# Kernel optimization log

Hardware: AMD Instinct MI355X
Metric: run time of the kernel (lower is better)

Reference implementation:

```python
import jax, jax.numpy as jnp
import numpy as np

N_GRIDS = 16
N_FEATS = 2
GRID_SHAPE = (64, 64, 64)  # D, H, W
NODES = 64
N_OUT = 1
DATA_MIN = 0.0
DATA_MAX = 1.0
N_POINTS = 524288


def setup_inputs() -> dict:
    key = jax.random.key(0)
    ks = jax.random.split(key, 12)
    x = jax.random.uniform(ks[0], (N_POINTS, 3), jnp.float32, -1.0, 1.0)
    # matches randomize_grids(): scales ~ log(1 - U*0.05), rotations ~ identity quat + noise,
    # translations ~ U(-0.05, 0.05)
    scales = jnp.log(1.0 - jax.random.uniform(ks[1], (N_GRIDS, 3), jnp.float32) * 0.05)
    rotations = jnp.zeros((N_GRIDS, 4), jnp.float32).at[:, 3].set(1.0) \
        + jax.random.normal(ks[2], (N_GRIDS, 4), jnp.float32) * 0.05
    translations = jax.random.uniform(ks[3], (N_GRIDS, 3), jnp.float32) * 0.1 - 0.05
    # original uses U(-1e-4, 1e-4); use a larger scale for numerically meaningful outputs
    feature_grids = jax.random.uniform(ks[4], (N_GRIDS, N_FEATS) + GRID_SHAPE,
                                       jnp.float32, -0.1, 0.1)
    d_in = N_GRIDS * N_FEATS
    def xavier(k, fi, fo):
        std = np.sqrt(2.0 / (fi + fo)).astype(np.float32)
        return jax.random.normal(k, (fi, fo), jnp.float32) * std
    W0 = xavier(ks[5], d_in, NODES)
    b0 = jax.random.normal(ks[6], (NODES,), jnp.float32) * 0.001
    W1 = xavier(ks[7], NODES, NODES)
    b1 = jax.random.normal(ks[8], (NODES,), jnp.float32) * 0.001
    W2 = xavier(ks[9], NODES, N_OUT)
    b2 = jax.random.normal(ks[10], (N_OUT,), jnp.float32) * 0.001
    return {"x": x, "rotations": rotations, "scales": scales,
            "translations": translations, "feature_grids": feature_grids,
            "W0": W0, "b0": b0, "W1": W1, "b1": b1, "W2": W2, "b2": b2}


def quat_to_rot(q):
    # q: [G,4] in (x, y, z, w) order; normalized (rotation_activation)
    q = q / jnp.linalg.norm(q, axis=-1, keepdims=True)
    x, y, z, w = q[:, 0], q[:, 1], q[:, 2], q[:, 3]
    r0 = jnp.stack([1 - 2 * (y * y + z * z), 2 * (x * y - z * w), 2 * (x * z + y * w)], -1)
    r1 = jnp.stack([2 * (x * y + z * w), 1 - 2 * (x * x + z * z), 2 * (y * z - x * w)], -1)
    r2 = jnp.stack([2 * (x * z - y * w), 2 * (y * z + x * w), 1 - 2 * (x * x + y * y)], -1)
    return jnp.stack([r0, r1, r2], axis=-2)  # [G,3,3]


def transform_points(x, rotations, scales, translations):
    # S*R*T order: local = diag(exp(scales)) @ R @ x + t, per grid -> [G,N,3]
    R = quat_to_rot(rotations)
    s = jnp.exp(scales)
    M = s[:, :, None] * R  # [G,3,3]
    return jnp.einsum('gij,nj->gni', M, x) + translations[:, None, :]


def trilinear_sample(grid, pts):
    # grid: [C,D,H,W]; pts: [N,3] (x,y,z) in [-1,1]; grid_sample semantics:
    # mode='bilinear', align_corners=True, padding_mode='zeros'
    C, D, H, W = grid.shape
    fx = (pts[:, 0] + 1.0) * 0.5 * (W - 1)
    fy = (pts[:, 1] + 1.0) * 0.5 * (H - 1)
    fz = (pts[:, 2] + 1.0) * 0.5 * (D - 1)
    x0 = jnp.floor(fx); y0 = jnp.floor(fy); z0 = jnp.floor(fz)
    wx = fx - x0; wy = fy - y0; wz = fz - z0
    x0i = x0.astype(jnp.int32); y0i = y0.astype(jnp.int32); z0i = z0.astype(jnp.int32)

    def corner(dx, dy, dz):
        xi = x0i + dx; yi = y0i + dy; zi = z0i + dz
        valid = (xi >= 0) & (xi < W) & (yi >= 0) & (yi < H) & (zi >= 0) & (zi < D)
        v = grid[:, jnp.clip(zi, 0, D - 1), jnp.clip(yi, 0, H - 1), jnp.clip(xi, 0, W - 1)]
        w = ((wx if dx else 1 - wx) * (wy if dy else 1 - wy) * (wz if dz else 1 - wz))
        return v * jnp.where(valid, w, 0.0)[None, :]

    out = corner(0, 0, 0)
    for dz in (0, 1):
        for dy in (0, 1):
            for dx in (0, 1):
                if (dx, dy, dz) != (0, 0, 0):
                    out = out + corner(dx, dy, dz)
    return out  # [C,N]


def reference(x, rotations, scales, translations, feature_grids, W0, b0, W1, b1, W2, b2):
    pts = transform_points(x, rotations, scales, translations)      # [G,N,3]
    feats = jax.vmap(trilinear_sample)(feature_grids, pts)          # [G,C,N]
    feats = feats.transpose(2, 0, 1).reshape(x.shape[0], -1)        # [N, G*C]
    h = jax.nn.relu(feats @ W0 + b0)
    h = jax.nn.relu(h @ W1 + b1)
    y = h @ W2 + b2
    return y * (DATA_MAX - DATA_MIN) + DATA_MIN
```

## Files before the change

### kernel.cpp

```cpp
#include <hip/hip_runtime.h>
#include <cstddef>
#include <cstdint>

constexpr int NPTS   = 524288;
constexpr int NG     = 16;
constexpr int GR     = 64;
constexpr int GR3    = GR * GR * GR;
constexpr int NNODES = 64;
constexpr int NBINS  = 32768;

constexpr size_t GRIDS_BYTES = (size_t)NG * GR3 * 8;
constexpr size_t WS_SORT     = GRIDS_BYTES;
constexpr size_t SORT_BYTES  = (size_t)NPTS * 16;
constexpr size_t WS_KEYR     = WS_SORT + SORT_BYTES;
constexpr size_t KEYR_BYTES  = (size_t)NPTS * 4;
constexpr size_t WS_BINS     = WS_KEYR + KEYR_BYTES;
constexpr size_t BINS_BYTES  = (size_t)NBINS * 4;
constexpr size_t WS_MATS     = WS_BINS + BINS_BYTES;
constexpr size_t MATS_BYTES  = 1024;
constexpr size_t WS_WPACK    = WS_MATS + MATS_BYTES;
constexpr size_t WPACK_BYTES = (size_t)(256 + 512) * 16;
constexpr size_t WS_PART     = WS_WPACK + WPACK_BYTES;
constexpr size_t PART_BYTES  = 128 * 4;
constexpr size_t WS_TOTAL    = WS_PART + PART_BYTES;

constexpr int PREP_REPACK = 4096;
constexpr int PREP_HIST   = 2048;

typedef _Float16 half8 __attribute__((ext_vector_type(8)));
typedef float    floatx4 __attribute__((ext_vector_type(4)));

__device__ __forceinline__ unsigned part1by2(unsigned x) {
    x &= 0x3ff;
    x = (x | (x << 16)) & 0x030000FF;
    x = (x | (x <<  8)) & 0x0300F00F;
    x = (x | (x <<  4)) & 0x030C30C3;
    x = (x | (x <<  2)) & 0x09249249;
    return x;
}

__device__ __forceinline__ unsigned cell_of(float px, float py, float pz) {
    int cx = (int)((px + 1.0f) * 16.0f); cx = min(max(cx, 0), 31);
    int cy = (int)((py + 1.0f) * 16.0f); cy = min(max(cy, 0), 31);
    int cz = (int)((pz + 1.0f) * 16.0f); cz = min(max(cz, 0), 31);
    return part1by2((unsigned)cx) | (part1by2((unsigned)cy) << 1) | (part1by2((unsigned)cz) << 2);
}

__device__ __forceinline__ unsigned f32_to_bf16_rne(float f) {
    unsigned u = __float_as_uint(f);
    return (u + 0x7fffu + ((u >> 16) & 1u)) >> 16;
}

__device__ __forceinline__ unsigned pack_h2(float a, float b) {
    unsigned short ua = __builtin_bit_cast(unsigned short, (_Float16)a);
    unsigned short ub = __builtin_bit_cast(unsigned short, (_Float16)b);
    return (unsigned)ua | ((unsigned)ub << 16);
}

__device__ __forceinline__ unsigned short f32_to_h16(float a) {
    return __builtin_bit_cast(unsigned short, (_Float16)a);
}

__global__ __launch_bounds__(256) void prep_kernel(
    const float* __restrict__ grids, uint2* __restrict__ gout,
    const float* __restrict__ xs, unsigned* __restrict__ bins,
    unsigned* __restrict__ keyrank,
    const float* __restrict__ rot, const float* __restrict__ scl,
    const float* __restrict__ trn, float* __restrict__ mats,
    const float* __restrict__ W0, const float* __restrict__ W1,
    uint4* __restrict__ wpack)
{
    const int bid = blockIdx.x;
    const int tid = threadIdx.x;

    if (bid < PREP_REPACK) {
        const int base = (bid * 256 + tid) * 4;
        const int g    = base >> 18;
        const int node = base & (GR3 - 1);
        const int x    = node & 63;
        const float* p0 = grids + (size_t)g * 2 * GR3 + node;
        const float* p1 = p0 + GR3;
        const float4 c0 = *(const float4*)p0;
        const float4 c1 = *(const float4*)p1;
        float d0n, d1n;
        if (x == 60) { d0n = c0.w; d1n = c1.w; }
        else         { d0n = p0[4]; d1n = p1[4]; }
        const float e0[5] = {c0.x, c0.y, c0.z, c0.w, d0n};
        const float e1[5] = {c1.x, c1.y, c1.z, c1.w, d1n};
        unsigned pk[5];
        #pragma unroll
        for (int i = 0; i < 5; ++i)
            pk[i] = f32_to_bf16_rne(e0[i]) | (f32_to_bf16_rne(e1[i]) << 16);
        uint4* dst = (uint4*)(gout + (size_t)g * GR3 + node);
        dst[0] = make_uint4(pk[0], pk[1], pk[1], pk[2]);
        dst[1] = make_uint4(pk[2], pk[3], pk[3], pk[4]);
    } else if (bid < PREP_REPACK + PREP_HIST) {
        const int n = (bid - PREP_REPACK) * 256 + tid;
        const unsigned key = cell_of(xs[n*3+0], xs[n*3+1], xs[n*3+2]);
        const unsigned rank = atomicAdd(&bins[key], 1u);
        keyrank[n] = key | (rank << 15);
    } else if (bid == PREP_REPACK + PREP_HIST) {
        const int g = tid;
        if (g < NG) {
            float qx = rot[g*4+0], qy = rot[g*4+1], qz = rot[g*4+2], qw = rot[g*4+3];
            const float inv = 1.0f / sqrtf(qx*qx + qy*qy + qz*qz + qw*qw);
            qx *= inv; qy *= inv; qz *= inv; qw *= inv;
            const float sx = expf(scl[g*3+0]);
            const float sy = expf(scl[g*3+1]);
            const float sz = expf(scl[g*3+2]);
            float* m = mats + g * 12;
            m[0] = sx * (1.0f - 2.0f*(qy*qy + qz*qz));
            m[1] = sx * (2.0f*(qx*qy - qz*qw));
            m[2] = sx * (2.0f*(qx*qz + qy*qw));
            m[3] = sy * (2.0f*(qx*qy + qz*qw));
            m[4] = sy * (1.0f - 2.0f*(qx*qx + qz*qz));
            m[5] = sy * (2.0f*(qy*qz - qx*qw));
            m[6] = sz * (2.0f*(qx*qz - qy*qw));
            m[7] = sz * (2.0f*(qy*qz + qx*qw));
            m[8] = sz * (1.0f - 2.0f*(qx*qx + qy*qy));
            m[9]  = trn[g*3+0];
            m[10] = trn[g*3+1];
            m[11] = trn[g*3+2];
        }
    } else {
        const int t = tid >> 6;
        const int lane = tid & 63;
        const int q = lane >> 4, c = lane & 15;
        const int n = t * 16 + c;
        {
            unsigned u[4];
            #pragma unroll
            for (int jj = 0; jj < 4; ++jj) {
                const int k0 = q * 8 + 2 * jj;
                u[jj] = pack_h2(W0[k0 * NNODES + n], W0[(k0 + 1) * NNODES + n]);
            }
            wpack[t * 64 + lane] = make_uint4(u[0], u[1], u[2], u[3]);
        }
        #pragma unroll
        for (int ks = 0; ks < 2; ++ks) {
            unsigned u[4];
            #pragma unroll
            for (int jj = 0; jj < 4; ++jj) {
                const int k0 = ks * 32 + q * 8 + 2 * jj;
                u[jj] = pack_h2(W1[k0 * NNODES + n], W1[(k0 + 1) * NNODES + n]);
            }
            wpack[256 + (ks * 4 + t) * 64 + lane] = make_uint4(u[0], u[1], u[2], u[3]);
        }
    }
}

__global__ __launch_bounds__(256) void scanA_kernel(unsigned* __restrict__ bins,
                                                    unsigned* __restrict__ part) {
    __shared__ unsigned s[256];
    const int t = threadIdx.x;
    const int base = blockIdx.x * 256;
    const unsigned v = bins[base + t];
    s[t] = v;
    __syncthreads();
    for (int off = 1; off < 256; off <<= 1) {
        unsigned u = (t >= off) ? s[t - off] : 0u;
        __syncthreads();
        s[t] += u;
        __syncthreads();
    }
    bins[base + t] = s[t] - v;
    if (t == 255) part[blockIdx.x] = s[255];
}

__global__ __launch_bounds__(128) void scanB_kernel(unsigned* __restrict__ part) {
    __shared__ unsigned s[128];
    const int t = threadIdx.x;
    const unsigned v = part[t];
    s[t] = v;
    __syncthreads();
    for (int off = 1; off < 128; off <<= 1) {
        unsigned u = (t >= off) ? s[t - off] : 0u;
        __syncthreads();
        s[t] += u;
        __syncthreads();
    }
    part[t] = s[t] - v;
}

__global__ __launch_bounds__(256) void scatter_kernel(const float* __restrict__ xs,
                                                      const unsigned* __restrict__ bins,
                                                      const unsigned* __restrict__ part,
                                                      const unsigned* __restrict__ keyrank,
                                                      float4* __restrict__ sorted) {
    const int n = blockIdx.x * 256 + threadIdx.x;
    if (n >= NPTS) return;
    const unsigned kr = keyrank[n];
    const unsigned key = kr & 0x7fffu;
    const unsigned rank = kr >> 15;
    const unsigned pos = part[key >> 8] + bins[key] + rank;
    sorted[pos] = make_float4(xs[n*3+0], xs[n*3+1], xs[n*3+2], __int_as_float(n));
}

struct Geom {
    unsigned i00, i01, i10, i11;
    float ax0, ax1, ay0, ay1, az0, az1;
};

__device__ __forceinline__ Geom make_geom(const float* __restrict__ m,
                                          float px, float py, float pz, int g) {
    Geom G;
    const float tx = fmaf(m[0], px, fmaf(m[1], py, fmaf(m[2], pz, m[9])));
    const float ty = fmaf(m[3], px, fmaf(m[4], py, fmaf(m[5], pz, m[10])));
    const float tz = fmaf(m[6], px, fmaf(m[7], py, fmaf(m[8], pz, m[11])));
    const float fx = (tx + 1.0f) * 31.5f;
    const float fy = (ty + 1.0f) * 31.5f;
    const float fz = (tz + 1.0f) * 31.5f;
    const float x0f = floorf(fx), y0f = floorf(fy), z0f = floorf(fz);
    const float wx = fx - x0f, wy = fy - y0f, wz = fz - z0f;
    const int x0 = (int)x0f, y0 = (int)y0f, z0 = (int)z0f;
    float ax0 = ((unsigned)x0       < 64u) ? (1.0f - wx) : 0.0f;
    float ax1 = ((unsigned)(x0 + 1) < 64u) ? wx          : 0.0f;
    const bool wrap = (x0 == -1);
    G.ax0 = wrap ? ax1 : ax0;
    G.ax1 = wrap ? 0.0f : ax1;
    G.ay0 = ((unsigned)y0       < 64u) ? (1.0f - wy) : 0.0f;
    G.ay1 = ((unsigned)(y0 + 1) < 64u) ? wy          : 0.0f;
    G.az0 = ((unsigned)z0       < 64u) ? (1.0f - wz) : 0.0f;
    G.az1 = ((unsigned)(z0 + 1) < 64u) ? wz          : 0.0f;
    const int xb  = min(max(x0, 0), 63);
    const int yc0 = min(max(y0, 0), 63),     yc1 = min(max(y0 + 1, 0), 63);
    const int zc0 = min(max(z0, 0), 63),     zc1 = min(max(z0 + 1, 0), 63);
    const unsigned b = (unsigned)(g << 18) + (unsigned)xb;
    G.i00 = b + (unsigned)((zc0 << 12) + (yc0 << 6));
    G.i01 = b + (unsigned)((zc0 << 12) + (yc1 << 6));
    G.i10 = b + (unsigned)((zc1 << 12) + (yc0 << 6));
    G.i11 = b + (unsigned)((zc1 << 12) + (yc1 << 6));
    return G;
}

__device__ __forceinline__ void acc_pair(float& f0, float& f1, const Geom& G,
                                         uint2 q, float wyz) {
    float s0 = G.ax0 * __uint_as_float(q.x << 16);
    s0 = fmaf(G.ax1, __uint_as_float(q.y << 16), s0);
    f0 = fmaf(wyz, s0, f0);
    float s1 = G.ax0 * __uint_as_float(q.x & 0xffff0000u);
    s1 = fmaf(G.ax1, __uint_as_float(q.y & 0xffff0000u), s1);
    f1 = fmaf(wyz, s1, f1);
}

constexpr int ARENA_H = 64 * 64;

__device__ __forceinline__ int sw_addr(int row, int halfcol) {
    return row * 64 + ((((halfcol >> 3) ^ (row & 7)) << 3) | (halfcol & 7));
}

__global__ __launch_bounds__(256, 4) void amgsrn_main(
    const float4* __restrict__ sorted,
    const uint2*  __restrict__ gridsP,
    const float*  __restrict__ mats,
    const uint4*  __restrict__ wpack,
    const float*  __restrict__ b0,
    const float*  __restrict__ b1,
    const float*  __restrict__ W2,
    const float*  __restrict__ b2,
    float* __restrict__ out)
{
    __shared__ unsigned short sh[4 * ARENA_H];

    const int tid  = threadIdx.x;
    const int lane = tid & 63;
    const int wv   = tid >> 6;
    const int c    = lane & 15;
    const int q    = lane >> 4;
    unsigned short* wa = sh + wv * ARENA_H;

    const int n = blockIdx.x * 256 + tid;
    const float4 p = sorted[n];
    const float px = p.x, py = p.y, pz = p.z;
    const int orig = __float_as_int(p.w);

    unsigned pk[NG];
    Geom Ga = make_geom(mats, px, py, pz, 0);
    uint2 a00 = gridsP[Ga.i00], a01 = gridsP[Ga.i01];
    uint2 a10 = gridsP[Ga.i10], a11 = gridsP[Ga.i11];
    Geom Gb = make_geom(mats + 12, px, py, pz, 1);
    uint2 b00 = gridsP[Gb.i00], b01 = gridsP[Gb.i01];
    uint2 b10 = gridsP[Gb.i10], b11 = gridsP[Gb.i11];
    #pragma unroll
    for (int g = 0; g < NG; ++g) {
        Geom Gn;
        uint2 n00, n01, n10, n11;
        if (g + 2 < NG) {
            Gn = make_geom(mats + (g + 2) * 12, px, py, pz, g + 2);
            n00 = gridsP[Gn.i00]; n01 = gridsP[Gn.i01];
            n10 = gridsP[Gn.i10]; n11 = gridsP[Gn.i11];
        }
        float f0 = 0.0f, f1 = 0.0f;
        acc_pair(f0, f1, Ga, a00, Ga.az0 * Ga.ay0);
        acc_pair(f0, f1, Ga, a01, Ga.az0 * Ga.ay1);
        acc_pair(f0, f1, Ga, a10, Ga.az1 * Ga.ay0);
        acc_pair(f0, f1, Ga, a11, Ga.az1 * Ga.ay1);
        pk[g] = pack_h2(f0, f1);
        Ga = Gb; a00 = b00; a01 = b01; a10 = b10; a11 = b11;
        if (g + 2 < NG) {
            Gb = Gn; b00 = n00; b01 = n01; b10 = n10; b11 = n11;
        }
    }

    #pragma unroll
    for (int g4 = 0; g4 < 4; ++g4)
        *(uint4*)(wa + sw_addr(lane, g4 * 8)) =
            make_uint4(pk[g4*4+0], pk[g4*4+1], pk[g4*4+2], pk[g4*4+3]);
    __syncthreads();

    half8 a0[4];
    #pragma unroll
    for (int m = 0; m < 4; ++m)
        a0[m] = *(const half8*)(wa + sw_addr(m * 16 + c, q * 8));

    half8 b0f[4], b1f[2][4];
    #pragma unroll
    for (int t = 0; t < 4; ++t)
        b0f[t] = __builtin_bit_cast(half8, wpack[t * 64 + lane]);
    #pragma unroll
    for (int ks = 0; ks < 2; ++ks)
        #pragma unroll
        for (int t = 0; t < 4; ++t)
            b1f[ks][t] = __builtin_bit_cast(half8, wpack[256 + (ks * 4 + t) * 64 + lane]);
    float b0v[4], b1v[4], w2v[4];
    #pragma unroll
    for (int t = 0; t < 4; ++t) {
        b0v[t] = b0[t * 16 + c];
        b1v[t] = b1[t * 16 + c];
        w2v[t] = W2[t * 16 + c];
    }
    const float b2s = b2[0];

    __syncthreads();

    #pragma unroll
    for (int t = 0; t < 4; ++t) {
        #pragma unroll
        for (int m = 0; m < 4; ++m) {
            floatx4 acc = {b0v[t], b0v[t], b0v[t], b0v[t]};
            acc = __builtin_amdgcn_mfma_f32_16x16x32_f16(a0[m], b0f[t], acc, 0, 0, 0);
            const int node = t * 16 + c;
            const int ptb  = m * 16 + q * 4;
            #pragma unroll
            for (int r = 0; r < 4; ++r)
                wa[sw_addr(ptb + r, node)] = f32_to_h16(fmaxf(acc[r], 0.0f));
        }
    }
    __syncthreads();

    half8 a1[4][2];
    #pragma unroll
    for (int m = 0; m < 4; ++m)
        #pragma unroll
        for (int ks = 0; ks < 2; ++ks)
            a1[m][ks] = *(const half8*)(wa + sw_addr(m * 16 + c, ks * 32 + q * 8));

    float p4[4][4];
    #pragma unroll
    for (int m = 0; m < 4; ++m)
        #pragma unroll
        for (int r = 0; r < 4; ++r) p4[m][r] = 0.0f;

    #pragma unroll
    for (int t = 0; t < 4; ++t) {
        #pragma unroll
        for (int m = 0; m < 4; ++m) {
            floatx4 acc = {b1v[t], b1v[t], b1v[t], b1v[t]};
            acc = __builtin_amdgcn_mfma_f32_16x16x32_f16(a1[m][0], b1f[0][t], acc, 0, 0, 0);
            acc = __builtin_amdgcn_mfma_f32_16x16x32_f16(a1[m][1], b1f[1][t], acc, 0, 0, 0);
            #pragma unroll
            for (int r = 0; r < 4; ++r)
                p4[m][r] = fmaf(fmaxf(acc[r], 0.0f), w2v[t], p4[m][r]);
        }
    }

    #pragma unroll
    for (int m = 0; m < 4; ++m)
        #pragma unroll
        for (int r = 0; r < 4; ++r) {
            float v = p4[m][r];
            v += __shfl_xor(v, 1, 64);
            v += __shfl_xor(v, 2, 64);
            v += __shfl_xor(v, 4, 64);
            v += __shfl_xor(v, 8, 64);
            p4[m][r] = v + b2s;
        }

    #pragma unroll
    for (int m = 0; m < 4; ++m)
        #pragma unroll
        for (int r = 0; r < 4; ++r) {
            const int srcPt = m * 16 + q * 4 + r;
            const int origPt = __shfl(orig, srcPt, 64);
            if (c == 0) out[origPt] = p4[m][r];
        }
}

__global__ __launch_bounds__(256, 3) void amgsrn_fused_fallback(
    const float* __restrict__ xs,
    const float* __restrict__ rot,
    const float* __restrict__ scl,
    const float* __restrict__ trn,
    const float* __restrict__ grids,
    const float* __restrict__ W0,
    const float* __restrict__ b0,
    const float* __restrict__ W1,
    const float* __restrict__ b1,
    const float* __restrict__ W2,
    const float* __restrict__ b2,
    float* __restrict__ out)
{
    __shared__ float sM[NG][12];
    const int tid = threadIdx.x;
    if (tid < NG) {
        const int g = tid;
        float qx = rot[g*4+0], qy = rot[g*4+1], qz = rot[g*4+2], qw = rot[g*4+3];
        const float inv = 1.0f / sqrtf(qx*qx + qy*qy + qz*qz + qw*qw);
        qx *= inv; qy *= inv; qz *= inv; qw *= inv;
        const float sx = expf(scl[g*3+0]);
        const float sy = expf(scl[g*3+1]);
        const float sz = expf(scl[g*3+2]);
        sM[g][0] = sx * (1.0f - 2.0f*(qy*qy + qz*qz));
        sM[g][1] = sx * (2.0f*(qx*qy - qz*qw));
        sM[g][2] = sx * (2.0f*(qx*qz + qy*qw));
        sM[g][3] = sy * (2.0f*(qx*qy + qz*qw));
        sM[g][4] = sy * (1.0f - 2.0f*(qx*qx + qz*qz));
        sM[g][5] = sy * (2.0f*(qy*qz - qx*qw));
        sM[g][6] = sz * (2.0f*(qx*qz - qy*qw));
        sM[g][7] = sz * (2.0f*(qy*qz + qx*qw));
        sM[g][8] = sz * (1.0f - 2.0f*(qx*qx + qy*qy));
        sM[g][9]  = trn[g*3+0];
        sM[g][10] = trn[g*3+1];
        sM[g][11] = trn[g*3+2];
    }
    __syncthreads();

    const int n = blockIdx.x * blockDim.x + tid;
    if (n >= NPTS) return;
    const float px = xs[n*3+0];
    const float py = xs[n*3+1];
    const float pz = xs[n*3+2];

    float h0[NNODES];
    #pragma unroll
    for (int j = 0; j < NNODES; ++j) h0[j] = b0[j];

    #pragma unroll
    for (int g = 0; g < NG; ++g) {
        const float* m = sM[g];
        const float tx = m[0]*px + m[1]*py + m[2]*pz + m[9];
        const float ty = m[3]*px + m[4]*py + m[5]*pz + m[10];
        const float tz = m[6]*px + m[7]*py + m[8]*pz + m[11];
        const float fx = (tx + 1.0f) * 31.5f;
        const float fy = (ty + 1.0f) * 31.5f;
        const float fz = (tz + 1.0f) * 31.5f;
        const float x0f = floorf(fx), y0f = floorf(fy), z0f = floorf(fz);
        const float wx = fx - x0f, wy = fy - y0f, wz = fz - z0f;
        const int x0 = (int)x0f, y0 = (int)y0f, z0 = (int)z0f;
        const float* gb = grids + (size_t)g * (size_t)(2 * GR3);
        float f0 = 0.0f, f1 = 0.0f;
        #pragma unroll
        for (int dz = 0; dz < 2; ++dz) {
            #pragma unroll
            for (int dy = 0; dy < 2; ++dy) {
                #pragma unroll
                for (int dx = 0; dx < 2; ++dx) {
                    const int xi = x0 + dx, yi = y0 + dy, zi = z0 + dz;
                    const bool valid = ((unsigned)xi < (unsigned)GR) &
                                       ((unsigned)yi < (unsigned)GR) &
                                       ((unsigned)zi < (unsigned)GR);
                    const int xc = min(max(xi, 0), GR-1);
                    const int yc = min(max(yi, 0), GR-1);
                    const int zc = min(max(zi, 0), GR-1);
                    float w = (dx ? wx : 1.0f - wx) *
                              (dy ? wy : 1.0f - wy) *
                              (dz ? wz : 1.0f - wz);
                    w = valid ? w : 0.0f;
                    const int idx = (zc * GR + yc) * GR + xc;
                    f0 = fmaf(w, gb[idx], f0);
                    f1 = fmaf(w, gb[idx + GR3], f1);
                }
            }
        }
        const float* w0a = W0 + (2*g    ) * NNODES;
        const float* w0b = W0 + (2*g + 1) * NNODES;
        #pragma unroll
        for (int j = 0; j < NNODES; ++j)
            h0[j] = fmaf(f1, w0b[j], fmaf(f0, w0a[j], h0[j]));
    }
    #pragma unroll
    for (int j = 0; j < NNODES; ++j) h0[j] = fmaxf(h0[j], 0.0f);

    float y = b2[0];
    #pragma unroll
    for (int half = 0; half < 2; ++half) {
        float h1[32];
        #pragma unroll
        for (int j = 0; j < 32; ++j) h1[j] = b1[half * 32 + j];
        #pragma unroll
        for (int k = 0; k < NNODES; ++k) {
            const float a = h0[k];
            const float* w = W1 + k * NNODES + half * 32;
            #pragma unroll
            for (int j = 0; j < 32; ++j) h1[j] = fmaf(a, w[j], h1[j]);
        }
        #pragma unroll
        for (int j = 0; j < 32; ++j) y = fmaf(fmaxf(h1[j], 0.0f), W2[half * 32 + j], y);
    }

    out[n] = y;
}

extern "C" void kernel_launch(void* const* d_in, const int* in_sizes, int n_in,
                              void* d_out, int out_size, void* d_ws, size_t ws_size,
                              hipStream_t stream) {
    const float* xs  = (const float*)d_in[0];
    const float* rot = (const float*)d_in[1];
    const float* scl = (const float*)d_in[2];
    const float* trn = (const float*)d_in[3];
    const float* gr  = (const float*)d_in[4];
    const float* W0  = (const float*)d_in[5];
    const float* b0  = (const float*)d_in[6];
    const float* W1  = (const float*)d_in[7];
    const float* b1  = (const float*)d_in[8];
    const float* W2  = (const float*)d_in[9];
    const float* b2  = (const float*)d_in[10];
    float* out = (float*)d_out;

    if (ws_size < WS_TOTAL) {
        dim3 grid((NPTS + 255) / 256), block(256);
        hipLaunchKernelGGL(amgsrn_fused_fallback, grid, block, 0, stream,
                           xs, rot, scl, trn, gr, W0, b0, W1, b1, W2, b2, out);
        return;
    }

    char* ws = (char*)d_ws;
    uint2*    gridsP  = (uint2*)(ws);
    float4*   sorted  = (float4*)(ws + WS_SORT);
    unsigned* keyrank = (unsigned*)(ws + WS_KEYR);
    unsigned* bins    = (unsigned*)(ws + WS_BINS);
    float*    mats    = (float*)(ws + WS_MATS);
    uint4*    wpack   = (uint4*)(ws + WS_WPACK);
    unsigned* part    = (unsigned*)(ws + WS_PART);

    hipMemsetAsync(bins, 0, BINS_BYTES, stream);
    hipLaunchKernelGGL(prep_kernel, dim3(PREP_REPACK + PREP_HIST + 2), dim3(256), 0, stream,
                       gr, gridsP, xs, bins, keyrank,
                       rot, scl, trn, mats, W0, W1, wpack);
    hipLaunchKernelGGL(scanA_kernel, dim3(NBINS / 256), dim3(256), 0, stream, bins, part);
    hipLaunchKernelGGL(scanB_kernel, dim3(1), dim3(128), 0, stream, part);
    hipLaunchKernelGGL(scatter_kernel, dim3(NPTS / 256), dim3(256), 0, stream,
                       xs, bins, part, keyrank, sorted);
    hipLaunchKernelGGL(amgsrn_main, dim3(NPTS / 256), dim3(256), 0, stream,
                       sorted, gridsP, mats, wpack, b0, b1, W2, b2, out);
}
```

Measured before the change: 192.8 us.

## Split fused gather+MLP into separate gather and MFMA MLP kernels

```diff
diff --git a/kernel.cpp b/kernel.cpp
--- a/kernel.cpp
+++ b/kernel.cpp
@@ -9,20 +9,15 @@
 constexpr int NNODES = 64;
 constexpr int NBINS  = 32768;
 
-constexpr size_t GRIDS_BYTES = (size_t)NG * GR3 * 8;
-constexpr size_t WS_SORT     = GRIDS_BYTES;
+constexpr size_t PAIR_GRIDS  = (size_t)NG * GR3 * 8;
+constexpr size_t FEATS_BYTES = (size_t)NPTS * 64;
 constexpr size_t SORT_BYTES  = (size_t)NPTS * 16;
-constexpr size_t WS_KEYR     = WS_SORT + SORT_BYTES;
 constexpr size_t KEYR_BYTES  = (size_t)NPTS * 4;
-constexpr size_t WS_BINS     = WS_KEYR + KEYR_BYTES;
 constexpr size_t BINS_BYTES  = (size_t)NBINS * 4;
-constexpr size_t WS_MATS     = WS_BINS + BINS_BYTES;
 constexpr size_t MATS_BYTES  = 1024;
-constexpr size_t WS_WPACK    = WS_MATS + MATS_BYTES;
 constexpr size_t WPACK_BYTES = (size_t)(256 + 512) * 16;
-constexpr size_t WS_PART     = WS_WPACK + WPACK_BYTES;
 constexpr size_t PART_BYTES  = 128 * 4;
-constexpr size_t WS_TOTAL    = WS_PART + PART_BYTES;
+constexpr size_t TAIL_BYTES  = SORT_BYTES + KEYR_BYTES + BINS_BYTES + MATS_BYTES + WPACK_BYTES + PART_BYTES;
 
 constexpr int PREP_REPACK = 4096;
 constexpr int PREP_HIST   = 2048;
@@ -60,6 +55,13 @@
 __device__ __forceinline__ unsigned short f32_to_h16(float a) {
     return __builtin_bit_cast(unsigned short, (_Float16)a);
 }
+
+__device__ __forceinline__ unsigned pack_b2(float a, float b) {
+    return f32_to_bf16_rne(a) | (f32_to_bf16_rne(b) << 16);
+}
+
+__device__ __forceinline__ float blo(unsigned u) { return __uint_as_float(u << 16); }
+__device__ __forceinline__ float bhi(unsigned u) { return __uint_as_float(u & 0xffff0000u); }
 
 __global__ __launch_bounds__(256) void prep_kernel(
     const float* __restrict__ grids, uint2* __restrict__ gout,
@@ -89,8 +91,7 @@
         const float e1[5] = {c1.x, c1.y, c1.z, c1.w, d1n};
         unsigned pk[5];
         #pragma unroll
-        for (int i = 0; i < 5; ++i)
-            pk[i] = f32_to_bf16_rne(e0[i]) | (f32_to_bf16_rne(e1[i]) << 16);
+        for (int i = 0; i < 5; ++i) pk[i] = pack_b2(e0[i], e1[i]);
         uint4* dst = (uint4*)(gout + (size_t)g * GR3 + node);
         dst[0] = make_uint4(pk[0], pk[1], pk[1], pk[2]);
         dst[1] = make_uint4(pk[2], pk[3], pk[3], pk[4]);
@@ -167,32 +168,28 @@
     if (t == 255) part[blockIdx.x] = s[255];
 }
 
-__global__ __launch_bounds__(128) void scanB_kernel(unsigned* __restrict__ part) {
-    __shared__ unsigned s[128];
-    const int t = threadIdx.x;
-    const unsigned v = part[t];
-    s[t] = v;
-    __syncthreads();
-    for (int off = 1; off < 128; off <<= 1) {
-        unsigned u = (t >= off) ? s[t - off] : 0u;
-        __syncthreads();
-        s[t] += u;
-        __syncthreads();
-    }
-    part[t] = s[t] - v;
-}
-
 __global__ __launch_bounds__(256) void scatter_kernel(const float* __restrict__ xs,
                                                       const unsigned* __restrict__ bins,
                                                       const unsigned* __restrict__ part,
                                                       const unsigned* __restrict__ keyrank,
                                                       float4* __restrict__ sorted) {
-    const int n = blockIdx.x * 256 + threadIdx.x;
-    if (n >= NPTS) return;
+    __shared__ unsigned sp[128];
+    const int t = threadIdx.x;
+    if (t < 128) sp[t] = part[t];
+    __syncthreads();
+    for (int off = 1; off < 128; off <<= 1) {
+        unsigned u = (t < 128 && t >= off) ? sp[t - off] : 0u;
+        __syncthreads();
+        if (t < 128) sp[t] += u;
+        __syncthreads();
+    }
+    const int n = blockIdx.x * 256 + t;
     const unsigned kr = keyrank[n];
     const unsigned key = kr & 0x7fffu;
     const unsigned rank = kr >> 15;
-    const unsigned pos = part[key >> 8] + bins[key] + rank;
+    const unsigned pidx = key >> 8;
+    const unsigned pbase = pidx ? sp[pidx - 1] : 0u;
+    const unsigned pos = pbase + bins[key] + rank;
     sorted[pos] = make_float4(xs[n*3+0], xs[n*3+1], xs[n*3+2], __int_as_float(n));
 }
 
@@ -235,12 +232,58 @@
 
 __device__ __forceinline__ void acc_pair(float& f0, float& f1, const Geom& G,
                                          uint2 q, float wyz) {
-    float s0 = G.ax0 * __uint_as_float(q.x << 16);
-    s0 = fmaf(G.ax1, __uint_as_float(q.y << 16), s0);
+    float s0 = G.ax0 * blo(q.x);
+    s0 = fmaf(G.ax1, blo(q.y), s0);
     f0 = fmaf(wyz, s0, f0);
-    float s1 = G.ax0 * __uint_as_float(q.x & 0xffff0000u);
-    s1 = fmaf(G.ax1, __uint_as_float(q.y & 0xffff0000u), s1);
+    float s1 = G.ax0 * bhi(q.x);
+    s1 = fmaf(G.ax1, bhi(q.y), s1);
     f1 = fmaf(wyz, s1, f1);
+}
+
+__global__ __launch_bounds__(256) void gather_kernel(
+    const float4* __restrict__ sorted,
+    const uint2*  __restrict__ gridsP,
+    const float*  __restrict__ mats,
+    uint4* __restrict__ feats)
+{
+    const int n = blockIdx.x * 256 + threadIdx.x;
+    const float4 p = sorted[n];
+    const float px = p.x, py = p.y, pz = p.z;
+
+    unsigned pk[NG];
+    Geom Ga = make_geom(mats, px, py, pz, 0);
+    uint2 a00 = gridsP[Ga.i00], a01 = gridsP[Ga.i01];
+    uint2 a10 = gridsP[Ga.i10], a11 = gridsP[Ga.i11];
+    Geom Gb = make_geom(mats + 12, px, py, pz, 1);
+    uint2 b00 = gridsP[Gb.i00], b01 = gridsP[Gb.i01];
+    uint2 b10 = gridsP[Gb.i10], b11 = gridsP[Gb.i11];
+    #pragma unroll
+    for (int g = 0; g < NG; ++g) {
+        Geom Gn;
+        uint2 n00, n01, n10, n11;
+        if (g + 2 < NG) {
+            Gn = make_geom(mats + (g + 2) * 12, px, py, pz, g + 2);
+            n00 = gridsP[Gn.i00]; n01 = gridsP[Gn.i01];
+            n10 = gridsP[Gn.i10]; n11 = gridsP[Gn.i11];
+        }
+        float f0 = 0.0f, f1 = 0.0f;
+        acc_pair(f0, f1, Ga, a00, Ga.az0 * Ga.ay0);
+        acc_pair(f0, f1, Ga, a01, Ga.az0 * Ga.ay1);
+        acc_pair(f0, f1, Ga, a10, Ga.az1 * Ga.ay0);
+        acc_pair(f0, f1, Ga, a11, Ga.az1 * Ga.ay1);
+        pk[g] = pack_h2(f0, f1);
+        Ga = Gb; a00 = b00; a01 = b01; a10 = b10; a11 = b11;
+        if (g + 2 < NG) {
+            Gb = Gn; b00 = n00; b01 = n01; b10 = n10; b11 = n11;
+        }
+    }
+
+    const int tile = n >> 6;
+    const int pt   = n & 63;
+    uint4* dst = feats + (size_t)tile * 256 + pt;
+    #pragma unroll
+    for (int g4 = 0; g4 < 4; ++g4)
+        dst[g4 * 64] = make_uint4(pk[g4*4+0], pk[g4*4+1], pk[g4*4+2], pk[g4*4+3]);
 }
 
 constexpr int ARENA_H = 64 * 64;
@@ -249,7 +292,116 @@
     return row * 64 + ((((halfcol >> 3) ^ (row & 7)) << 3) | (halfcol & 7));
 }
 
-__global__ __launch_bounds__(256, 4) void amgsrn_main(
+__global__ __launch_bounds__(256, 4) void mlp_kernel(
+    const float4* __restrict__ sorted,
+    const uint4*  __restrict__ feats,
+    const uint4*  __restrict__ wpack,
+    const float*  __restrict__ b0,
+    const float*  __restrict__ b1,
+    const float*  __restrict__ W2,
+    const float*  __restrict__ b2,
+    float* __restrict__ out)
+{
+    __shared__ unsigned short sh[4 * ARENA_H];
+
+    const int tid  = threadIdx.x;
+    const int lane = tid & 63;
+    const int wv   = tid >> 6;
+    const int c    = lane & 15;
+    const int q    = lane >> 4;
+    unsigned short* wa = sh + wv * ARENA_H;
+
+    const int n = blockIdx.x * 256 + tid;
+    const int orig = __float_as_int(sorted[n].w);
+    const uint4* fb = feats + (size_t)(blockIdx.x * 4 + wv) * 256;
+
+    half8 a0[4];
+    #pragma unroll
+    for (int m = 0; m < 4; ++m)
+        a0[m] = __builtin_bit_cast(half8, fb[q * 64 + m * 16 + c]);
+
+    half8 b0f[4], b1f[2][4];
+    #pragma unroll
+    for (int t = 0; t < 4; ++t)
+        b0f[t] = __builtin_bit_cast(half8, wpack[t * 64 + lane]);
+    #pragma unroll
+    for (int ks = 0; ks < 2; ++ks)
+        #pragma unroll
+        for (int t = 0; t < 4; ++t)
+            b1f[ks][t] = __builtin_bit_cast(half8, wpack[256 + (ks * 4 + t) * 64 + lane]);
+    float b0v[4], b1v[4], w2v[4];
+    #pragma unroll
+    for (int t = 0; t < 4; ++t) {
+        b0v[t] = b0[t * 16 + c];
+        b1v[t] = b1[t * 16 + c];
+        w2v[t] = W2[t * 16 + c];
+    }
+    const float b2s = b2[0];
+
+    #pragma unroll
+    for (int t = 0; t < 4; ++t) {
+        #pragma unroll
+        for (int m = 0; m < 4; ++m) {
+            floatx4 acc = {b0v[t], b0v[t], b0v[t], b0v[t]};
+            acc = __builtin_amdgcn_mfma_f32_16x16x32_f16(a0[m], b0f[t], acc, 0, 0, 0);
+            const int node = t * 16 + c;
+            const int ptb  = m * 16 + q * 4;
+            #pragma unroll
+            for (int r = 0; r < 4; ++r)
+                wa[sw_addr(ptb + r, node)] = f32_to_h16(fmaxf(acc[r], 0.0f));
+        }
+    }
+    __syncthreads();
+
+    half8 a1[4][2];
+    #pragma unroll
+    for (int m = 0; m < 4; ++m)
+        #pragma unroll
+        for (int ks = 0; ks < 2; ++ks)
+            a1[m][ks] = *(const half8*)(wa + sw_addr(m * 16 + c, ks * 32 + q * 8));
+
+    float p4[4][4];
+    #pragma unroll
+    for (int m = 0; m < 4; ++m)
+        #pragma unroll
+        for (int r = 0; r < 4; ++r) p4[m][r] = 0.0f;
+
+    #pragma unroll
+    for (int t = 0; t < 4; ++t) {
+        #pragma unroll
+        for (int m = 0; m < 4; ++m) {
+            floatx4 acc = {b1v[t], b1v[t], b1v[t], b1v[t]};
+            acc = __builtin_amdgcn_mfma_f32_16x16x32_f16(a1[m][0], b1f[0][t], acc, 0, 0, 0);
+            acc = __builtin_amdgcn_mfma_f32_16x16x32_f16(a1[m][1], b1f[1][t], acc, 0, 0, 0);
+            #pragma unroll
+            for (int r = 0; r < 4; ++r)
+                p4[m][r] = fmaf(fmaxf(acc[r], 0.0f), w2v[t], p4[m][r]);
+        }
+    }
+
+    #pragma unroll
+    for (int m = 0; m < 4; ++m)
+        #pragma unroll
+        for (int r = 0; r < 4; ++r) {
+            float v = p4[m][r];
+            v += __shfl_xor(v, 1, 64);
+            v += __shfl_xor(v, 2, 64);
+            v += __shfl_xor(v, 4, 64);
+            v += __shfl_xor(v, 8, 64);
+            p4[m][r] = v + b2s;
+        }
+
+    #pragma unroll
+    for (int m = 0; m < 4; ++m)
+        #pragma unroll
+        for (int r = 0; r < 4; ++r) {
+            const int srcPt = m * 16 + q * 4 + r;
+            const int origPt = __shfl(orig, srcPt, 64);
+            if (c == 0) out[origPt] = p4[m][r];
+        }
+}
+
+__global__ __launch_bounds__(256, 4) void amgsrn_main_pair(
     const float4* __restrict__ sorted,
     const uint2*  __restrict__ gridsP,
     const float*  __restrict__ mats,
@@ -527,7 +679,9 @@
     const float* b2  = (const float*)d_in[10];
     float* out = (float*)d_out;
 
-    if (ws_size < WS_TOTAL) {
+    const bool split = (ws_size >= PAIR_GRIDS + FEATS_BYTES + TAIL_BYTES);
+    const bool mono  = (ws_size >= PAIR_GRIDS + TAIL_BYTES);
+    if (!split && !mono) {
         dim3 grid((NPTS + 255) / 256), block(256);
         hipLaunchKernelGGL(amgsrn_fused_fallback, grid, block, 0, stream,
                            xs, rot, scl, trn, gr, W0, b0, W1, b1, W2, b2, out);
@@ -535,22 +689,31 @@
     }
 
     char* ws = (char*)d_ws;
-    uint2*    gridsP  = (uint2*)(ws);
-    float4*   sorted  = (float4*)(ws + WS_SORT);
-    unsigned* keyrank = (unsigned*)(ws + WS_KEYR);
-    unsigned* bins    = (unsigned*)(ws + WS_BINS);
-    float*    mats    = (float*)(ws + WS_MATS);
-    uint4*    wpack   = (uint4*)(ws + WS_WPACK);
-    unsigned* part    = (unsigned*)(ws + WS_PART);
+    uint2* gridsP = (uint2*)ws;
+    size_t off = PAIR_GRIDS;
+    uint4* feats = nullptr;
+    if (split) { feats = (uint4*)(ws + off); off += FEATS_BYTES; }
+    float4*   sorted  = (float4*)(ws + off);                 off += SORT_BYTES;
+    unsigned* keyrank = (unsigned*)(ws + off);               off += KEYR_BYTES;
+    unsigned* bins    = (unsigned*)(ws + off);               off += BINS_BYTES;
+    float*    mats    = (float*)(ws + off);                  off += MATS_BYTES;
+    uint4*    wpack   = (uint4*)(ws + off);                  off += WPACK_BYTES;
+    unsigned* part    = (unsigned*)(ws + off);
 
     hipMemsetAsync(bins, 0, BINS_BYTES, stream);
     hipLaunchKernelGGL(prep_kernel, dim3(PREP_REPACK + PREP_HIST + 2), dim3(256), 0, stream,
                        gr, gridsP, xs, bins, keyrank,
                        rot, scl, trn, mats, W0, W1, wpack);
     hipLaunchKernelGGL(scanA_kernel, dim3(NBINS / 256), dim3(256), 0, stream, bins, part);
-    hipLaunchKernelGGL(scanB_kernel, dim3(1), dim3(128), 0, stream, part);
     hipLaunchKernelGGL(scatter_kernel, dim3(NPTS / 256), dim3(256), 0, stream,
                        xs, bins, part, keyrank, sorted);
-    hipLaunchKernelGGL(amgsrn_main, dim3(NPTS / 256), dim3(256), 0, stream,
-                       sorted, gridsP, mats, wpack, b0, b1, W2, b2, out);
-}
+    if (split) {
+        hipLaunchKernelGGL(gather_kernel, dim3(NPTS / 256), dim3(256), 0, stream,
+                           sorted, gridsP, mats, feats);
+        hipLaunchKernelGGL(mlp_kernel, dim3(NPTS / 256), dim3(256), 0, stream,
+                           sorted, feats, wpack, b0, b1, W2, b2, out);
+    } else {
+        hipLaunchKernelGGL(amgsrn_main_pair, dim3(NPTS / 256), dim3(256), 0, stream,
+                           sorted, gridsP, mats, wpack, b0, b1, W2, b2, out);
+    }
+}
```

After: 199.3 us. 3.4% more time.
